# Optimization experiments

Hardware: AMD Instinct MI355X
Metric: run time of the kernel (lower is better)

Reference implementation:

```python
import jax, jax.numpy as jnp
import numpy as np

B, L, H = 4, 512, 768
S, R = 100, 100          # num spans, num relations
E = 25                   # size embedding dim
MAXLEN = 100             # max entity length (size embedding vocab)
NE, NR = 10, 6           # entity / relation type counts
NEG = jnp.float32(-1e20)


def _span_masks(key, batch, n, seqlen, max_len):
    k1, k2 = jax.random.split(key)
    starts = jax.random.randint(k1, (batch, n), 0, seqlen - max_len)
    lens = jax.random.randint(k2, (batch, n), 1, max_len)
    pos = jnp.arange(seqlen)
    m = (pos[None, None, :] >= starts[..., None]) & (pos[None, None, :] < (starts + lens)[..., None])
    return m.astype(jnp.int32)  # (batch, n, seqlen), contiguous 0/1 spans


def setup_inputs() -> dict:
    key = jax.random.key(0)
    ks = jax.random.split(key, 8)
    hidden_states = jax.random.normal(ks[0], (B, L, H), dtype=jnp.float32)
    entity_masks = _span_masks(ks[1], B, S, L, 20)            # span len < MAXLEN
    relation_context_masks = _span_masks(ks[2], B, R, L, 50)  # context len < MAXLEN
    relations = jax.random.randint(ks[3], (B, R, 2), 0, S)
    size_emb = jax.random.normal(ks[4], (MAXLEN, E), dtype=jnp.float32) * 0.02
    w_span = jax.random.normal(ks[5], (E + H, NE), dtype=jnp.float32) * 0.02
    b_span = jnp.zeros((NE,), dtype=jnp.float32)
    w_rel = jax.random.normal(ks[6], (2 * E + 3 * H, NR), dtype=jnp.float32) * 0.02
    b_rel = jnp.zeros((NR,), dtype=jnp.float32)
    return {
        'hidden_states': hidden_states,
        'entity_masks': entity_masks,
        'relations': relations,
        'relation_context_masks': relation_context_masks,
        'size_emb': size_emb,
        'w_span': w_span,
        'b_span': b_span,
        'w_rel': w_rel,
        'b_rel': b_rel,
    }


def _masked_max(hidden, masks):
    # hidden: (B, L, H); masks: (B, N, L) 0/1 -> (B, N, H) max over masked positions
    # Matches torch: h.unsqueeze(1)*m then masked_fill(m==0, -1e20), max over L
    masked = jnp.where(masks[..., None] != 0, hidden[:, None, :, :], NEG)
    return jnp.max(masked, axis=-2)


def reference(hidden_states, entity_masks, relations, relation_context_masks,
              size_emb, w_span, b_span, w_rel, b_rel):
    # entity sizes -> size embedding lookup
    entity_sizes = size_emb[entity_masks.sum(-1)]                     # (B, S, E)

    # entity span max-pool + classify
    entities = _masked_max(hidden_states, entity_masks)               # (B, S, H)
    entity_reprs = jnp.concatenate([entities, entity_sizes], axis=-1)
    entity_logits = entity_reprs @ w_span + b_span                    # (B, S, NE)

    # relation context max-pool
    rel_ctx = _masked_max(hidden_states, relation_context_masks)      # (B, R, H)

    # gather entity pairs
    b, r = relations.shape[:2]
    rel_flat = relations.reshape(b, -1)                               # (B, 2R)
    pairs = jnp.take_along_axis(entities, rel_flat[:, :, None], axis=1).reshape(b, r, -1)
    pair_sizes = jnp.take_along_axis(entity_sizes, rel_flat[:, :, None], axis=1).reshape(b, r, -1)

    rel_reprs = jnp.concatenate([rel_ctx, pairs, pair_sizes], axis=-1)
    relation_logits = rel_reprs @ w_rel + b_rel                       # (B, R, NR)
    return entity_logits, relation_logits
```

## Files before the change

### kernel.cpp

```cpp
#include <hip/hip_runtime.h>

#define B 4
#define L 512
#define H 768
#define S 100
#define R 100
#define E 25
#define NE 10
#define NR 6
#define NEGF (-1e20f)

__device__ __forceinline__ void mask_stats_partial(
    const int* __restrict__ mrow, int t, int wave, int lane,
    int (*sc)[4], int (*sm)[4], int k)
{
    int c = 0, mn = L;
    #pragma unroll
    for (int i = 0; i < 2; ++i) {
        const int l = t + i * 256;
        const int m = mrow[l];
        c += (m != 0);
        if (m != 0 && l < mn) mn = l;
    }
    for (int off = 32; off > 0; off >>= 1) {
        c += __shfl_down(c, off, 64);
        mn = min(mn, __shfl_down(mn, off, 64));
    }
    if (lane == 0) { sc[k][wave] = c; sm[k][wave] = mn; }
}

__device__ __forceinline__ void span_pool(
    const float* __restrict__ hb, int start, int n,
    int h0, int h1, int h2, float& mv0, float& mv1, float& mv2)
{
    mv0 = NEGF; mv1 = NEGF; mv2 = NEGF;
    const float* hp = hb + (size_t)start * H;
    for (int i = 0; i < n; ++i, hp += H) {
        mv0 = fmaxf(mv0, hp[h0]);
        mv1 = fmaxf(mv1, hp[h1]);
        mv2 = fmaxf(mv2, hp[h2]);
    }
}

__global__ __launch_bounds__(256) void spert_fused_kernel(
    const float* __restrict__ hidden,
    const int*   __restrict__ emask,
    const int*   __restrict__ relations,
    const int*   __restrict__ cmask,
    const float* __restrict__ size_emb,
    const float* __restrict__ w_span,
    const float* __restrict__ b_span,
    const float* __restrict__ w_rel,
    const float* __restrict__ b_rel,
    float* __restrict__ ent_logits,
    float* __restrict__ rel_logits)
{
    const int idx  = blockIdx.x;
    const int b    = idx / (S + R);
    const int j    = idx % (S + R);
    const int t    = threadIdx.x;
    const int wave = t >> 6;
    const int lane = t & 63;
    const int h0 = t, h1 = t + 256, h2 = t + 512;

    __shared__ int   sc[3][4], sm[3][4];
    __shared__ float sred[4][NE];

    const float* hb = hidden + (size_t)b * L * H;

    if (j < S) {
        const int* mrow = emask + (size_t)(b * S + j) * L;
        mask_stats_partial(mrow, t, wave, lane, sc, sm, 0);
        __syncthreads();
        const int n     = sc[0][0] + sc[0][1] + sc[0][2] + sc[0][3];
        const int start = min(min(sm[0][0], sm[0][1]), min(sm[0][2], sm[0][3]));

        float mv0, mv1, mv2;
        span_pool(hb, start, n, h0, h1, h2, mv0, mv1, mv2);

        float p[NE];
        #pragma unroll
        for (int o = 0; o < NE; ++o)
            p[o] = mv0 * w_span[(size_t)h0 * NE + o]
                 + mv1 * w_span[(size_t)h1 * NE + o]
                 + mv2 * w_span[(size_t)h2 * NE + o];
        if (t < E) {
            const float sz = size_emb[(size_t)n * E + t];
            #pragma unroll
            for (int o = 0; o < NE; ++o) p[o] += sz * w_span[(size_t)(H + t) * NE + o];
        }
        #pragma unroll
        for (int o = 0; o < NE; ++o) {
            float v = p[o];
            for (int off = 32; off > 0; off >>= 1) v += __shfl_down(v, off, 64);
            p[o] = v;
        }
        if (lane == 0) {
            #pragma unroll
            for (int o = 0; o < NE; ++o) sred[wave][o] = p[o];
        }
        __syncthreads();
        if (t < NE) {
            const float v = sred[0][t] + sred[1][t] + sred[2][t] + sred[3][t] + b_span[t];
            ent_logits[(size_t)(b * S + j) * NE + t] = v;
        }
    } else {
        const int r    = j - S;
        const int head = relations[(size_t)(b * R + r) * 2 + 0];
        const int tail = relations[(size_t)(b * R + r) * 2 + 1];

        mask_stats_partial(cmask + (size_t)(b * R + r)    * L, t, wave, lane, sc, sm, 0);
        mask_stats_partial(emask + (size_t)(b * S + head) * L, t, wave, lane, sc, sm, 1);
        mask_stats_partial(emask + (size_t)(b * S + tail) * L, t, wave, lane, sc, sm, 2);
        __syncthreads();

        int n[3], st[3];
        #pragma unroll
        for (int k = 0; k < 3; ++k) {
            n[k]  = sc[k][0] + sc[k][1] + sc[k][2] + sc[k][3];
            st[k] = min(min(sm[k][0], sm[k][1]), min(sm[k][2], sm[k][3]));
        }

        float mv[3][3];
        #pragma unroll
        for (int k = 0; k < 3; ++k)
            span_pool(hb, st[k], n[k], h0, h1, h2, mv[k][0], mv[k][1], mv[k][2]);

        float p[NR];
        #pragma unroll
        for (int o = 0; o < NR; ++o)
            p[o] = mv[0][0] * w_rel[(size_t) h0          * NR + o]
                 + mv[0][1] * w_rel[(size_t) h1          * NR + o]
                 + mv[0][2] * w_rel[(size_t) h2          * NR + o]
                 + mv[1][0] * w_rel[(size_t)(H + h0)     * NR + o]
                 + mv[1][1] * w_rel[(size_t)(H + h1)     * NR + o]
                 + mv[1][2] * w_rel[(size_t)(H + h2)     * NR + o]
                 + mv[2][0] * w_rel[(size_t)(2 * H + h0) * NR + o]
                 + mv[2][1] * w_rel[(size_t)(2 * H + h1) * NR + o]
                 + mv[2][2] * w_rel[(size_t)(2 * H + h2) * NR + o];
        if (t < E) {
            const float sz = size_emb[(size_t)n[1] * E + t];
            #pragma unroll
            for (int o = 0; o < NR; ++o) p[o] += sz * w_rel[(size_t)(3 * H + t) * NR + o];
        } else if (t >= 32 && t < 32 + E) {
            const int e = t - 32;
            const float sz = size_emb[(size_t)n[2] * E + e];
            #pragma unroll
            for (int o = 0; o < NR; ++o) p[o] += sz * w_rel[(size_t)(3 * H + E + e) * NR + o];
        }

        #pragma unroll
        for (int o = 0; o < NR; ++o) {
            float v = p[o];
            for (int off = 32; off > 0; off >>= 1) v += __shfl_down(v, off, 64);
            p[o] = v;
        }
        if (lane == 0) {
            #pragma unroll
            for (int o = 0; o < NR; ++o) sred[wave][o] = p[o];
        }
        __syncthreads();
        if (t < NR) {
            const float v = sred[0][t] + sred[1][t] + sred[2][t] + sred[3][t] + b_rel[t];
            rel_logits[(size_t)(b * R + r) * NR + t] = v;
        }
    }
}

extern "C" void kernel_launch(void* const* d_in, const int* in_sizes, int n_in,
                              void* d_out, int out_size, void* d_ws, size_t ws_size,
                              hipStream_t stream) {
    const float* hidden    = (const float*)d_in[0];
    const int*   emask     = (const int*)  d_in[1];
    const int*   relations = (const int*)  d_in[2];
    const int*   cmask     = (const int*)  d_in[3];
    const float* size_emb  = (const float*)d_in[4];
    const float* w_span    = (const float*)d_in[5];
    const float* b_span    = (const float*)d_in[6];
    const float* w_rel     = (const float*)d_in[7];
    const float* b_rel     = (const float*)d_in[8];

    float* out        = (float*)d_out;
    float* ent_logits = out;
    float* rel_logits = out + B * S * NE;

    spert_fused_kernel<<<B * (S + R), 256, 0, stream>>>(
        hidden, emask, relations, cmask, size_emb,
        w_span, b_span, w_rel, b_rel, ent_logits, rel_logits);
}
```

Measured before the change: 94.65 us.

## Split into pooling and relation kernels to stop recomputing entity max-pools

New measurement: 93.20 us. No clear change (-1.5%).

```diff
diff --git a/kernel.cpp b/kernel.cpp
--- a/kernel.cpp
+++ b/kernel.cpp
@@ -9,15 +9,14 @@
 #define NE 10
 #define NR 6
 #define NEGF (-1e20f)
+#define TPB 192
 
-__device__ __forceinline__ void mask_stats_partial(
-    const int* __restrict__ mrow, int t, int wave, int lane,
-    int (*sc)[4], int (*sm)[4], int k)
+__device__ __forceinline__ void mask_stats(const int* __restrict__ mrow,
+                                           int t, int wave, int lane,
+                                           int* sc, int* sm, int& n, int& start)
 {
     int c = 0, mn = L;
-    #pragma unroll
-    for (int i = 0; i < 2; ++i) {
-        const int l = t + i * 256;
+    for (int l = t; l < L; l += TPB) {
         const int m = mrow[l];
         c += (m != 0);
         if (m != 0 && l < mn) mn = l;
@@ -26,34 +25,56 @@
         c += __shfl_down(c, off, 64);
         mn = min(mn, __shfl_down(mn, off, 64));
     }
-    if (lane == 0) { sc[k][wave] = c; sm[k][wave] = mn; }
+    if (lane == 0) { sc[wave] = c; sm[wave] = mn; }
+    __syncthreads();
+    n = sc[0] + sc[1] + sc[2];
+    start = min(min(sm[0], sm[1]), sm[2]);
 }
 
-__device__ __forceinline__ void span_pool(
-    const float* __restrict__ hb, int start, int n,
-    int h0, int h1, int h2, float& mv0, float& mv1, float& mv2)
+__device__ __forceinline__ float4 span_pool4(const float* __restrict__ hb,
+                                             int start, int n, int t)
 {
-    mv0 = NEGF; mv1 = NEGF; mv2 = NEGF;
-    const float* hp = hb + (size_t)start * H;
-    for (int i = 0; i < n; ++i, hp += H) {
-        mv0 = fmaxf(mv0, hp[h0]);
-        mv1 = fmaxf(mv1, hp[h1]);
-        mv2 = fmaxf(mv2, hp[h2]);
+    float4 mv = make_float4(NEGF, NEGF, NEGF, NEGF);
+    const float4* hp = reinterpret_cast<const float4*>(hb + (size_t)start * H) + t;
+    for (int i = 0; i < n; ++i, hp += H / 4) {
+        const float4 v = *hp;
+        mv.x = fmaxf(mv.x, v.x); mv.y = fmaxf(mv.y, v.y);
+        mv.z = fmaxf(mv.z, v.z); mv.w = fmaxf(mv.w, v.w);
     }
+    return mv;
 }
 
-__global__ __launch_bounds__(256) void spert_fused_kernel(
+template <int NO>
+__device__ __forceinline__ void block_reduce_store(float* p, int t, int wave, int lane,
+                                                   float (*sred)[NO],
+                                                   const float* __restrict__ bias,
+                                                   float* __restrict__ outrow)
+{
+    #pragma unroll
+    for (int o = 0; o < NO; ++o) {
+        float v = p[o];
+        for (int off = 32; off > 0; off >>= 1) v += __shfl_down(v, off, 64);
+        p[o] = v;
+    }
+    if (lane == 0) {
+        #pragma unroll
+        for (int o = 0; o < NO; ++o) sred[wave][o] = p[o];
+    }
+    __syncthreads();
+    if (t < NO) outrow[t] = sred[0][t] + sred[1][t] + sred[2][t] + bias[t];
+}
+
+__global__ __launch_bounds__(TPB) void pool_kernel(
     const float* __restrict__ hidden,
     const int*   __restrict__ emask,
-    const int*   __restrict__ relations,
     const int*   __restrict__ cmask,
     const float* __restrict__ size_emb,
     const float* __restrict__ w_span,
     const float* __restrict__ b_span,
-    const float* __restrict__ w_rel,
-    const float* __restrict__ b_rel,
-    float* __restrict__ ent_logits,
-    float* __restrict__ rel_logits)
+    float* __restrict__ entities,
+    int*   __restrict__ n_ent,
+    float* __restrict__ rel_ctx,
+    float* __restrict__ ent_logits)
 {
     const int idx  = blockIdx.x;
     const int b    = idx / (S + R);
@@ -61,110 +82,88 @@
     const int t    = threadIdx.x;
     const int wave = t >> 6;
     const int lane = t & 63;
-    const int h0 = t, h1 = t + 256, h2 = t + 512;
 
-    __shared__ int   sc[3][4], sm[3][4];
-    __shared__ float sred[4][NE];
+    __shared__ int   sc[3], sm[3];
+    __shared__ float sred[3][NE];
 
     const float* hb = hidden + (size_t)b * L * H;
+    const int* mrow = (j < S) ? (emask + (size_t)(b * S + j) * L)
+                              : (cmask + (size_t)(b * R + (j - S)) * L);
+    int n, start;
+    mask_stats(mrow, t, wave, lane, sc, sm, n, start);
 
-    if (j < S) {
-        const int* mrow = emask + (size_t)(b * S + j) * L;
-        mask_stats_partial(mrow, t, wave, lane, sc, sm, 0);
-        __syncthreads();
-        const int n     = sc[0][0] + sc[0][1] + sc[0][2] + sc[0][3];
-        const int start = min(min(sm[0][0], sm[0][1]), min(sm[0][2], sm[0][3]));
+    const float4 mv = span_pool4(hb, start, n, t);
 
-        float mv0, mv1, mv2;
-        span_pool(hb, start, n, h0, h1, h2, mv0, mv1, mv2);
+    if (j >= S) {
+        reinterpret_cast<float4*>(rel_ctx + (size_t)(b * R + (j - S)) * H)[t] = mv;
+        return;
+    }
 
-        float p[NE];
+    reinterpret_cast<float4*>(entities + (size_t)(b * S + j) * H)[t] = mv;
+    if (t == 0) n_ent[b * S + j] = n;
+
+    float p[NE];
+    const float* w0 = w_span + (size_t)(4 * t) * NE;
+    #pragma unroll
+    for (int o = 0; o < NE; ++o)
+        p[o] = mv.x * w0[o] + mv.y * w0[NE + o] + mv.z * w0[2 * NE + o] + mv.w * w0[3 * NE + o];
+    if (t < E) {
+        const float sz = size_emb[(size_t)n * E + t];
         #pragma unroll
-        for (int o = 0; o < NE; ++o)
-            p[o] = mv0 * w_span[(size_t)h0 * NE + o]
-                 + mv1 * w_span[(size_t)h1 * NE + o]
-                 + mv2 * w_span[(size_t)h2 * NE + o];
-        if (t < E) {
-            const float sz = size_emb[(size_t)n * E + t];
-            #pragma unroll
-            for (int o = 0; o < NE; ++o) p[o] += sz * w_span[(size_t)(H + t) * NE + o];
-        }
+        for (int o = 0; o < NE; ++o) p[o] += sz * w_span[(size_t)(H + t) * NE + o];
+    }
+    block_reduce_store<NE>(p, t, wave, lane, sred, b_span,
+                           ent_logits + (size_t)(b * S + j) * NE);
+}
+
+__global__ __launch_bounds__(TPB) void rel_kernel(
+    const float* __restrict__ entities,
+    const int*   __restrict__ n_ent,
+    const float* __restrict__ rel_ctx,
+    const int*   __restrict__ relations,
+    const float* __restrict__ size_emb,
+    const float* __restrict__ w_rel,
+    const float* __restrict__ b_rel,
+    float* __restrict__ rel_logits)
+{
+    const int idx  = blockIdx.x;
+    const int b    = idx / R;
+    const int r    = idx % R;
+    const int t    = threadIdx.x;
+    const int wave = t >> 6;
+    const int lane = t & 63;
+
+    const int head = relations[(size_t)(b * R + r) * 2 + 0];
+    const int tail = relations[(size_t)(b * R + r) * 2 + 1];
+
+    const float4 c4 = reinterpret_cast<const float4*>(rel_ctx  + (size_t)(b * R + r)    * H)[t];
+    const float4 h4 = reinterpret_cast<const float4*>(entities + (size_t)(b * S + head) * H)[t];
+    const float4 t4 = reinterpret_cast<const float4*>(entities + (size_t)(b * S + tail) * H)[t];
+
+    float p[NR];
+    const float* wc = w_rel + (size_t)(4 * t) * NR;
+    const float* wh = w_rel + (size_t)(H + 4 * t) * NR;
+    const float* wt = w_rel + (size_t)(2 * H + 4 * t) * NR;
+    #pragma unroll
+    for (int o = 0; o < NR; ++o)
+        p[o] = c4.x * wc[o] + c4.y * wc[NR + o] + c4.z * wc[2 * NR + o] + c4.w * wc[3 * NR + o]
+             + h4.x * wh[o] + h4.y * wh[NR + o] + h4.z * wh[2 * NR + o] + h4.w * wh[3 * NR + o]
+             + t4.x * wt[o] + t4.y * wt[NR + o] + t4.z * wt[2 * NR + o] + t4.w * wt[3 * NR + o];
+
+    if (t < E) {
+        const float sz = size_emb[(size_t)n_ent[b * S + head] * E + t];
         #pragma unroll
-        for (int o = 0; o < NE; ++o) {
-            float v = p[o];
-            for (int off = 32; off > 0; off >>= 1) v += __shfl_down(v, off, 64);
-            p[o] = v;
-        }
-        if (lane == 0) {
-            #pragma unroll
-            for (int o = 0; o < NE; ++o) sred[wave][o] = p[o];
-        }
-        __syncthreads();
-        if (t < NE) {
-            const float v = sred[0][t] + sred[1][t] + sred[2][t] + sred[3][t] + b_span[t];
-            ent_logits[(size_t)(b * S + j) * NE + t] = v;
-        }
-    } else {
-        const int r    = j - S;
-        const int head = relations[(size_t)(b * R + r) * 2 + 0];
-        const int tail = relations[(size_t)(b * R + r) * 2 + 1];
+        for (int o = 0; o < NR; ++o) p[o] += sz * w_rel[(size_t)(3 * H + t) * NR + o];
+    } else if (t >= 64 && t < 64 + E) {
+        const int e = t - 64;
+        const float sz = size_emb[(size_t)n_ent[b * S + tail] * E + e];
+        #pragma unroll
+        for (int o = 0; o < NR; ++o) p[o] += sz * w_rel[(size_t)(3 * H + E + e) * NR + o];
+    }
 
-        mask_stats_partial(cmask + (size_t)(b * R + r)    * L, t, wave, lane, sc, sm, 0);
-        mask_stats_partial(emask + (size_t)(b * S + head) * L, t, wave, lane, sc, sm, 1);
-        mask_stats_partial(emask + (size_t)(b * S + tail) * L, t, wave, lane, sc, sm, 2);
-        __syncthreads();
-
-        int n[3], st[3];
-        #pragma unroll
-        for (int k = 0; k < 3; ++k) {
-            n[k]  = sc[k][0] + sc[k][1] + sc[k][2] + sc[k][3];
-            st[k] = min(min(sm[k][0], sm[k][1]), min(sm[k][2], sm[k][3]));
-        }
-
-        float mv[3][3];
-        #pragma unroll
-        for (int k = 0; k < 3; ++k)
-            span_pool(hb, st[k], n[k], h0, h1, h2, mv[k][0], mv[k][1], mv[k][2]);
-
-        float p[NR];
-        #pragma unroll
-        for (int o = 0; o < NR; ++o)
-            p[o] = mv[0][0] * w_rel[(size_t) h0          * NR + o]
-                 + mv[0][1] * w_rel[(size_t) h1          * NR + o]
-                 + mv[0][2] * w_rel[(size_t) h2          * NR + o]
-                 + mv[1][0] * w_rel[(size_t)(H + h0)     * NR + o]
-                 + mv[1][1] * w_rel[(size_t)(H + h1)     * NR + o]
-                 + mv[1][2] * w_rel[(size_t)(H + h2)     * NR + o]
-                 + mv[2][0] * w_rel[(size_t)(2 * H + h0) * NR + o]
-                 + mv[2][1] * w_rel[(size_t)(2 * H + h1) * NR + o]
-                 + mv[2][2] * w_rel[(size_t)(2 * H + h2) * NR + o];
-        if (t < E) {
-            const float sz = size_emb[(size_t)n[1] * E + t];
-            #pragma unroll
-            for (int o = 0; o < NR; ++o) p[o] += sz * w_rel[(size_t)(3 * H + t) * NR + o];
-        } else if (t >= 32 && t < 32 + E) {
-            const int e = t - 32;
-            const float sz = size_emb[(size_t)n[2] * E + e];
-            #pragma unroll
-            for (int o = 0; o < NR; ++o) p[o] += sz * w_rel[(size_t)(3 * H + E + e) * NR + o];
-        }
-
-        #pragma unroll
-        for (int o = 0; o < NR; ++o) {
-            float v = p[o];
-            for (int off = 32; off > 0; off >>= 1) v += __shfl_down(v, off, 64);
-            p[o] = v;
-        }
-        if (lane == 0) {
-            #pragma unroll
-            for (int o = 0; o < NR; ++o) sred[wave][o] = p[o];
-        }
-        __syncthreads();
-        if (t < NR) {
-            const float v = sred[0][t] + sred[1][t] + sred[2][t] + sred[3][t] + b_rel[t];
-            rel_logits[(size_t)(b * R + r) * NR + t] = v;
-        }
-    }
+    __shared__ float sred[3][NR];
+    block_reduce_store<NR>(p, t, wave, lane, sred, b_rel,
+                           rel_logits + (size_t)(b * R + r) * NR);
 }
 
 extern "C" void kernel_launch(void* const* d_in, const int* in_sizes, int n_in,
@@ -184,7 +183,15 @@
     float* ent_logits = out;
     float* rel_logits = out + B * S * NE;
 
-    spert_fused_kernel<<<B * (S + R), 256, 0, stream>>>(
-        hidden, emask, relations, cmask, size_emb,
-        w_span, b_span, w_rel, b_rel, ent_logits, rel_logits);
+    float* ws       = (float*)d_ws;
+    float* entities = ws;
+    float* rel_ctx  = entities + (size_t)B * S * H;
+    int*   n_ent    = (int*)(rel_ctx + (size_t)B * R * H);
+
+    pool_kernel<<<B * (S + R), TPB, 0, stream>>>(
+        hidden, emask, cmask, size_emb, w_span, b_span,
+        entities, n_ent, rel_ctx, ent_logits);
+
+    rel_kernel<<<B * R, TPB, 0, stream>>>(
+        entities, n_ent, rel_ctx, relations, size_emb, w_rel, b_rel, rel_logits);
 }
```
